# Optimization experiments

Hardware: AMD Instinct MI355X
Metric: run time of the kernel (lower is better)

The kernel has to match this reference:

```python
import jax, jax.numpy as jnp
import numpy as np

N = 2_000_000   # total nodes across all DAGs in the batch
M = 20_000      # number of DAGs
F = 8           # num_node_features
E = 32          # embed_dim
H = 64          # mlp hidden dim


def setup_inputs() -> dict:
    key = jax.random.key(0)
    ks = jax.random.split(key, 9)
    x = jax.random.normal(ks[0], (N, F), jnp.float32)
    h_node = jax.random.normal(ks[1], (N, E), jnp.float32)
    # CSR pointer: monotone, ptr[0]=0, ptr[-1]=N  -> M ragged segments
    inner = jnp.sort(jax.random.randint(ks[2], (M - 1,), 0, N, dtype=jnp.int32))
    ptr = jnp.concatenate([jnp.zeros((1,), jnp.int32), inner,
                           jnp.full((1,), N, jnp.int32)])
    # MLP params (Linear layers, Kaiming-ish scale)
    W1 = jax.random.normal(ks[3], (F + E, H), jnp.float32) / np.sqrt(F + E)
    b1 = jnp.zeros((H,), jnp.float32)
    W2 = jax.random.normal(ks[4], (H, H), jnp.float32) / np.sqrt(H)
    b2 = jnp.zeros((H,), jnp.float32)
    W3 = jax.random.normal(ks[5], (H, E), jnp.float32) / np.sqrt(H)
    b3 = jnp.zeros((E,), jnp.float32)
    return {"x": x, "h_node": h_node, "W1": W1, "b1": b1, "W2": W2,
            "b2": b2, "W3": W3, "b3": b3, "ptr": ptr}


def reference(x, h_node, W1, b1, W2, b2, W3, b3, ptr):
    # concat node feats with incoming node embeddings: [N, F+E]
    h = jnp.concatenate([x, h_node], axis=1)
    # MLP: Linear->ReLU->Linear->ReLU->Linear  (make_mlp with hid_dims=[64,64])
    h = jax.nn.relu(h @ W1 + b1)
    h = jax.nn.relu(h @ W2 + b2)
    h = h @ W3 + b3                      # [N, E]
    # segment_csr(reduce='sum') over ragged DAG groups defined by ptr
    counts = jnp.diff(ptr)               # [M] segment lengths
    seg_ids = jnp.repeat(jnp.arange(M, dtype=jnp.int32), counts,
                         total_repeat_length=N)
    return jax.ops.segment_sum(h, seg_ids, num_segments=M)  # [M, E]
```

## Files before the change

### kernel.cpp

```cpp
#include <hip/hip_runtime.h>

#define BLOCK 256
#define NPB 64
#define NF 8
#define NE 32
#define NI 40
#define NH 64
#define LDSW 65

typedef float fvec16 __attribute__((ext_vector_type(16)));
typedef float fvec8  __attribute__((ext_vector_type(8)));

__global__ __launch_bounds__(BLOCK, 4) void dag_mlp_seg(
    const float* __restrict__ x, const float* __restrict__ h_node,
    const float* __restrict__ W1, const float* __restrict__ b1,
    const float* __restrict__ W2, const float* __restrict__ b2,
    const float* __restrict__ W3, const float* __restrict__ b3,
    const int* __restrict__ ptr, float* __restrict__ out,
    int n, int m)
{
    __shared__ float sA[NPB * LDSW];
    __shared__ float sB[NPB * LDSW];

    const int tid = threadIdx.x;
    const int nd  = tid & 63;
    const int g   = __builtin_amdgcn_readfirstlane(tid >> 6);
    const long long node0 = (long long)blockIdx.x * NPB;

    {
        const long long x4max  = ((long long)n * NF) / 4 - 1;
        const long long h4max  = ((long long)n * NE) / 4 - 1;
        if (tid < 128) {
            long long gi = node0 * (NF / 4) + tid;
            if (gi > x4max) gi = x4max;
            float4 v = reinterpret_cast<const float4*>(x)[gi];
            const int nd2 = tid >> 1, c = (tid & 1) * 4;
            float* p = &sA[nd2 * LDSW + c];
            p[0] = v.x; p[1] = v.y; p[2] = v.z; p[3] = v.w;
        }
#pragma unroll
        for (int r = 0; r < 2; ++r) {
            const int j = tid + r * BLOCK;
            long long gi = node0 * (NE / 4) + j;
            if (gi > h4max) gi = h4max;
            float4 v = reinterpret_cast<const float4*>(h_node)[gi];
            const int nd2 = j >> 3, c = (j & 7) * 4;
            float* p = &sA[nd2 * LDSW + NF + c];
            p[0] = v.x; p[1] = v.y; p[2] = v.z; p[3] = v.w;
        }
    }
    __syncthreads();

    float acc[16];
    {
        fvec16 bv = *reinterpret_cast<const fvec16*>(b1 + g * 16);
#pragma unroll
        for (int c = 0; c < 16; ++c) acc[c] = bv[c];
        const float* inRow = &sA[nd * LDSW];
#pragma unroll 8
        for (int k = 0; k < NI; ++k) {
            const float s = inRow[k];
            fvec16 w = *reinterpret_cast<const fvec16*>(W1 + k * NH + g * 16);
#pragma unroll
            for (int c = 0; c < 16; ++c) acc[c] = fmaf(s, w[c], acc[c]);
        }
        float* o = &sB[nd * LDSW + g * 16];
#pragma unroll
        for (int c = 0; c < 16; ++c) o[c] = fmaxf(acc[c], 0.f);
    }
    __syncthreads();

    {
        fvec16 bv = *reinterpret_cast<const fvec16*>(b2 + g * 16);
#pragma unroll
        for (int c = 0; c < 16; ++c) acc[c] = bv[c];
        const float* inRow = &sB[nd * LDSW];
#pragma unroll 8
        for (int k = 0; k < NH; ++k) {
            const float s = inRow[k];
            fvec16 w = *reinterpret_cast<const fvec16*>(W2 + k * NH + g * 16);
#pragma unroll
            for (int c = 0; c < 16; ++c) acc[c] = fmaf(s, w[c], acc[c]);
        }
        float* o = &sA[nd * LDSW + g * 16];
#pragma unroll
        for (int c = 0; c < 16; ++c) o[c] = fmaxf(acc[c], 0.f);
    }
    __syncthreads();

    float ov[8];
    {
        fvec8 bv = *reinterpret_cast<const fvec8*>(b3 + g * 8);
#pragma unroll
        for (int c = 0; c < 8; ++c) ov[c] = bv[c];
        const float* inRow = &sA[nd * LDSW];
#pragma unroll 8
        for (int k = 0; k < NH; ++k) {
            const float s = inRow[k];
            fvec8 w = *reinterpret_cast<const fvec8*>(W3 + k * NE + g * 8);
#pragma unroll
            for (int c = 0; c < 8; ++c) ov[c] = fmaf(s, w[c], ov[c]);
        }
    }

    const long long node = node0 + nd;
    const bool valid = node < n;
    int seg = -1;
    if (valid) {
        int lo = 0, hi = m;
        while (hi - lo > 1) {
            int mid = (lo + hi) >> 1;
            if (ptr[mid] <= (int)node) lo = mid; else hi = mid;
        }
        seg = lo;
    }

    const int lane = nd;
    const int segUp = __shfl_up(seg, 1);
    const bool head = (lane == 0) || (segUp != seg);

    bool take[6];
#pragma unroll
    for (int i = 0; i < 6; ++i) {
        const int d = 1 << i;
        const int s2 = __shfl_down(seg, d);
        take[i] = (lane + d < 64) && (s2 == seg);
    }

#pragma unroll
    for (int j = 0; j < 8; ++j) {
        float v = valid ? ov[j] : 0.f;
#pragma unroll
        for (int i = 0; i < 6; ++i) {
            const float w = __shfl_down(v, 1 << i);
            if (take[i]) v += w;
        }
        if (head && seg >= 0) {
            atomicAdd(&out[(size_t)seg * NE + g * 8 + j], v);
        }
    }
}

extern "C" void kernel_launch(void* const* d_in, const int* in_sizes, int n_in,
                              void* d_out, int out_size, void* d_ws, size_t ws_size,
                              hipStream_t stream) {
    const float* x      = (const float*)d_in[0];
    const float* h_node = (const float*)d_in[1];
    const float* W1     = (const float*)d_in[2];
    const float* b1     = (const float*)d_in[3];
    const float* W2     = (const float*)d_in[4];
    const float* b2     = (const float*)d_in[5];
    const float* W3     = (const float*)d_in[6];
    const float* b3     = (const float*)d_in[7];
    const int*   ptr    = (const int*)d_in[8];
    float* out = (float*)d_out;

    const int n = in_sizes[0] / NF;
    const int m = out_size / NE;

    hipMemsetAsync(d_out, 0, (size_t)out_size * sizeof(float), stream);

    const int nb = (n + NPB - 1) / NPB;
    dag_mlp_seg<<<nb, BLOCK, 0, stream>>>(x, h_node, W1, b1, W2, b2, W3, b3,
                                          ptr, out, n, m);
}
```

Measured before the change: 822.2 us.

## Precompute per-block segment starts, shrink LDS, and raise occupancy target

Adds a small pre-kernel that binary-searches ptr once per 64-node block into workspace. The main kernel then walks forward linearly from that start instead of doing a full per-node binary search. LDS use drops by narrowing sA to 41 columns and reusing sB for layer-2 output, which needs an extra barrier. Launch bounds rise from 4 to 6 blocks per CU to improve latency hiding, at the risk of register spills and of long linear walks when a block spans many tiny segments.

```diff
diff --git a/kernel.cpp b/kernel.cpp
--- a/kernel.cpp
+++ b/kernel.cpp
@@ -6,21 +6,38 @@
 #define NE 32
 #define NI 40
 #define NH 64
-#define LDSW 65
+#define SA_W 41
+#define SB_W 65
 
 typedef float fvec16 __attribute__((ext_vector_type(16)));
 typedef float fvec8  __attribute__((ext_vector_type(8)));
 
-__global__ __launch_bounds__(BLOCK, 4) void dag_mlp_seg(
+__global__ void seg_starts(const int* __restrict__ ptr, int* __restrict__ blockseg,
+                           int nb, int n, int m)
+{
+    int b = blockIdx.x * blockDim.x + threadIdx.x;
+    if (b >= nb) return;
+    long long n0 = (long long)b * NPB;
+    int node0 = (int)(n0 < n ? n0 : (long long)(n - 1));
+    int lo = 0, hi = m;
+    while (hi - lo > 1) {
+        int mid = (lo + hi) >> 1;
+        if (ptr[mid] <= node0) lo = mid; else hi = mid;
+    }
+    blockseg[b] = lo;
+}
+
+template<bool PRESEG>
+__global__ __launch_bounds__(BLOCK, 6) void dag_mlp_seg(
     const float* __restrict__ x, const float* __restrict__ h_node,
     const float* __restrict__ W1, const float* __restrict__ b1,
     const float* __restrict__ W2, const float* __restrict__ b2,
     const float* __restrict__ W3, const float* __restrict__ b3,
     const int* __restrict__ ptr, float* __restrict__ out,
-    int n, int m)
+    const int* __restrict__ blockseg, int n, int m)
 {
-    __shared__ float sA[NPB * LDSW];
-    __shared__ float sB[NPB * LDSW];
+    __shared__ float sA[NPB * SA_W];
+    __shared__ float sB[NPB * SB_W];
 
     const int tid = threadIdx.x;
     const int nd  = tid & 63;
@@ -35,7 +52,7 @@
             if (gi > x4max) gi = x4max;
             float4 v = reinterpret_cast<const float4*>(x)[gi];
             const int nd2 = tid >> 1, c = (tid & 1) * 4;
-            float* p = &sA[nd2 * LDSW + c];
+            float* p = &sA[nd2 * SA_W + c];
             p[0] = v.x; p[1] = v.y; p[2] = v.z; p[3] = v.w;
         }
 #pragma unroll
@@ -45,7 +62,7 @@
             if (gi > h4max) gi = h4max;
             float4 v = reinterpret_cast<const float4*>(h_node)[gi];
             const int nd2 = j >> 3, c = (j & 7) * 4;
-            float* p = &sA[nd2 * LDSW + NF + c];
+            float* p = &sA[nd2 * SA_W + NF + c];
             p[0] = v.x; p[1] = v.y; p[2] = v.z; p[3] = v.w;
         }
     }
@@ -56,7 +73,7 @@
         fvec16 bv = *reinterpret_cast<const fvec16*>(b1 + g * 16);
 #pragma unroll
         for (int c = 0; c < 16; ++c) acc[c] = bv[c];
-        const float* inRow = &sA[nd * LDSW];
+        const float* inRow = &sA[nd * SA_W];
 #pragma unroll 8
         for (int k = 0; k < NI; ++k) {
             const float s = inRow[k];
@@ -64,7 +81,7 @@
 #pragma unroll
             for (int c = 0; c < 16; ++c) acc[c] = fmaf(s, w[c], acc[c]);
         }
-        float* o = &sB[nd * LDSW + g * 16];
+        float* o = &sB[nd * SB_W + g * 16];
 #pragma unroll
         for (int c = 0; c < 16; ++c) o[c] = fmaxf(acc[c], 0.f);
     }
@@ -74,7 +91,7 @@
         fvec16 bv = *reinterpret_cast<const fvec16*>(b2 + g * 16);
 #pragma unroll
         for (int c = 0; c < 16; ++c) acc[c] = bv[c];
-        const float* inRow = &sB[nd * LDSW];
+        const float* inRow = &sB[nd * SB_W];
 #pragma unroll 8
         for (int k = 0; k < NH; ++k) {
             const float s = inRow[k];
@@ -82,7 +99,10 @@
 #pragma unroll
             for (int c = 0; c < 16; ++c) acc[c] = fmaf(s, w[c], acc[c]);
         }
-        float* o = &sA[nd * LDSW + g * 16];
+    }
+    __syncthreads();
+    {
+        float* o = &sB[nd * SB_W + g * 16];
 #pragma unroll
         for (int c = 0; c < 16; ++c) o[c] = fmaxf(acc[c], 0.f);
     }
@@ -93,7 +113,7 @@
         fvec8 bv = *reinterpret_cast<const fvec8*>(b3 + g * 8);
 #pragma unroll
         for (int c = 0; c < 8; ++c) ov[c] = bv[c];
-        const float* inRow = &sA[nd * LDSW];
+        const float* inRow = &sB[nd * SB_W];
 #pragma unroll 8
         for (int k = 0; k < NH; ++k) {
             const float s = inRow[k];
@@ -105,15 +125,20 @@
 
     const long long node = node0 + nd;
     const bool valid = node < n;
-    int seg = -1;
-    if (valid) {
+    const int nodeC = (int)(valid ? node : (long long)(n - 1));
+    int seg;
+    if constexpr (PRESEG) {
+        seg = blockseg[blockIdx.x];
+    } else {
+        const int node0C = (int)(node0 < n ? node0 : (long long)(n - 1));
         int lo = 0, hi = m;
         while (hi - lo > 1) {
             int mid = (lo + hi) >> 1;
-            if (ptr[mid] <= (int)node) lo = mid; else hi = mid;
+            if (ptr[mid] <= node0C) lo = mid; else hi = mid;
         }
         seg = lo;
     }
+    while (seg + 1 < m && ptr[seg + 1] <= nodeC) ++seg;
 
     const int lane = nd;
     const int segUp = __shfl_up(seg, 1);
@@ -135,7 +160,7 @@
             const float w = __shfl_down(v, 1 << i);
             if (take[i]) v += w;
         }
-        if (head && seg >= 0) {
+        if (head && valid) {
             atomicAdd(&out[(size_t)seg * NE + g * 8 + j], v);
         }
     }
@@ -161,6 +186,15 @@
     hipMemsetAsync(d_out, 0, (size_t)out_size * sizeof(float), stream);
 
     const int nb = (n + NPB - 1) / NPB;
-    dag_mlp_seg<<<nb, BLOCK, 0, stream>>>(x, h_node, W1, b1, W2, b2, W3, b3,
-                                          ptr, out, n, m);
+    const bool preseg = (d_ws != nullptr) && (ws_size >= (size_t)nb * sizeof(int));
+
+    if (preseg) {
+        int* blockseg = (int*)d_ws;
+        seg_starts<<<(nb + 255) / 256, 256, 0, stream>>>(ptr, blockseg, nb, n, m);
+        dag_mlp_seg<true><<<nb, BLOCK, 0, stream>>>(x, h_node, W1, b1, W2, b2, W3, b3,
+                                                    ptr, out, blockseg, n, m);
+    } else {
+        dag_mlp_seg<false><<<nb, BLOCK, 0, stream>>>(x, h_node, W1, b1, W2, b2, W3, b3,
+                                                     ptr, out, nullptr, n, m);
+    }
 }
```

Measured after the change: 719.4 us. -12.5%, faster.
